# Optimization experiments

Measured on AMD Instinct MI355X. Metric: run time of the kernel, lower is better.

## Reference

```python
import jax, jax.numpy as jnp
import numpy as np


def _gcn_conv(x, edge_index, W, b):
    """Faithful PyG GCNConv: add self-loops, symmetric norm, scatter-sum, bias."""
    n = x.shape[0]
    loop = jnp.arange(n, dtype=edge_index.dtype)
    src = jnp.concatenate([edge_index[0], loop])  # [E+n]
    dst = jnp.concatenate([edge_index[1], loop])
    # in-degree at dst (edge_weight = 1), as in gcn_norm
    deg = jax.ops.segment_sum(jnp.ones(src.shape[0], x.dtype), dst, num_segments=n)
    dinv = jnp.where(deg > 0, jax.lax.rsqrt(deg), 0.0)
    norm = dinv[src] * dinv[dst]                  # [E+n]
    h = x @ W                                     # [n, C] small GEMM
    msg = h[src] * norm[:, None]                  # gather + scale (dominant traffic)
    out = jax.ops.segment_sum(msg, dst, num_segments=n)  # scatter-sum
    return out + b


def setup_inputs() -> dict:
    key = jax.random.key(0)
    ks = jax.random.split(key, 8)
    N, E, C = 50000, 1000000, 64
    scale = 1.0 / np.sqrt(C)
    return {
        "x_star": jax.random.normal(ks[0], (N, C), jnp.float32),
        "x_gal": jax.random.normal(ks[1], (N, C), jnp.float32),
        "edge_ss_near": jax.random.randint(ks[2], (2, E), 0, N, jnp.int64),
        "edge_ss_far": jax.random.randint(ks[3], (2, E), 0, N, jnp.int64),
        "edge_gg_near": jax.random.randint(ks[4], (2, E), 0, N, jnp.int64),
        "W_ss_near": jax.random.normal(ks[5], (C, C), jnp.float32) * scale,
        "W_ss_far": jax.random.normal(ks[6], (C, C), jnp.float32) * scale,
        "W_gg_near": jax.random.normal(ks[7], (C, C), jnp.float32) * scale,
        "b_ss_near": jnp.zeros((C,), jnp.float32),
        "b_ss_far": jnp.zeros((C,), jnp.float32),
        "b_gg_near": jnp.zeros((C,), jnp.float32),
    }


def reference(x_star, x_gal, edge_ss_near, edge_ss_far, edge_gg_near,
              W_ss_near, W_ss_far, W_gg_near,
              b_ss_near, b_ss_far, b_gg_near):
    # HeteroConv with aggr='sum': per-edge-type GCNConv, summed per dst node type.
    out_star = (_gcn_conv(x_star, edge_ss_near, W_ss_near, b_ss_near)
                + _gcn_conv(x_star, edge_ss_far, W_ss_far, b_ss_far))
    out_gal = _gcn_conv(x_gal, edge_gg_near, W_gg_near, b_gg_near)
    return out_star, out_gal
```

## Files before the change

### kernel.cpp

```cpp
#include <hip/hip_runtime.h>
#include <hip/hip_fp16.h>

#define CCH 64
#define RPB 32
#define PCH 8192
#define NBMAX 1568
#define GR 64
#define SG 8
#define STCAP 8192

typedef int int4a __attribute__((ext_vector_type(4), aligned(4)));

__global__ void __launch_bounds__(256) k_hist(const int* __restrict__ e0,
        const int* __restrict__ e1, const int* __restrict__ e2,
        int* __restrict__ H, int* __restrict__ cnt, int E, int NB, int NBLK) {
    int c = blockIdx.y;
    const int* dd = ((c == 0) ? e0 : (c == 1) ? e1 : e2) + E;
    int base = blockIdx.x * PCH;
    int nE = E - base; if (nE > PCH) nE = PCH;
    __shared__ int hist[NBMAX];
    int t = threadIdx.x;
    for (int i = t; i < NB; i += 256) hist[i] = 0;
    __syncthreads();
    for (int k = t * 4; k < nE; k += 1024) {
        if (k + 3 < nE) {
            int4a d = *(const int4a*)(dd + base + k);
            atomicAdd(&hist[d.x >> 5], 1); atomicAdd(&hist[d.y >> 5], 1);
            atomicAdd(&hist[d.z >> 5], 1); atomicAdd(&hist[d.w >> 5], 1);
        } else {
            for (int j = k; j < nE; ++j) atomicAdd(&hist[dd[base + j] >> 5], 1);
        }
    }
    __syncthreads();
    int* Hrow = H + ((size_t)c * NBLK + blockIdx.x) * NB;
    for (int i = t; i < NB; i += 256) {
        int h = hist[i];
        Hrow[i] = h;
        if (h) atomicAdd(&cnt[c * NB + i], h);
    }
}

__global__ void __launch_bounds__(1024) k_bscan(const int* __restrict__ cnt,
        int* __restrict__ bstart, __half* __restrict__ zrow, int NB, int E) {
    int c = blockIdx.x, t = threadIdx.x;
    if (c == 0 && t < 32) ((float*)zrow)[t] = 0.f;
    __shared__ int sm[1024];
    int i0 = 2 * t, i1 = 2 * t + 1;
    int v0 = (i0 < NB) ? cnt[c * NB + i0] : 0;
    int v1 = (i1 < NB) ? cnt[c * NB + i1] : 0;
    sm[t] = v0 + v1;
    __syncthreads();
    #pragma unroll
    for (int off = 1; off < 1024; off <<= 1) {
        int u = (t >= off) ? sm[t - off] : 0;
        __syncthreads();
        sm[t] += u;
        __syncthreads();
    }
    int ex = sm[t] - (v0 + v1);
    if (i0 < NB) bstart[c * (NB + 1) + i0] = ex;
    if (i1 < NB) bstart[c * (NB + 1) + i1] = ex + v0;
    if (t == 0) bstart[c * (NB + 1) + NB] = E;
}

__global__ void __launch_bounds__(256) k_colscan(int* __restrict__ H,
        const int* __restrict__ bstart, int NB, int NBLK) {
    int c = blockIdx.y;
    int b = blockIdx.x * 4 + (threadIdx.x >> 6);
    if (b >= NB) return;
    int l = threadIdx.x & 63;
    int* Hc = H + (size_t)c * NBLK * NB;
    int run = bstart[c * (NB + 1) + b];
    for (int c0 = 0; c0 < NBLK; c0 += 64) {
        int blk = c0 + l;
        int v = (blk < NBLK) ? Hc[(size_t)blk * NB + b] : 0;
        int s = v;
        #pragma unroll
        for (int off = 1; off < 64; off <<= 1) {
            int u = __shfl_up(s, off, 64);
            if (l >= off) s += u;
        }
        if (blk < NBLK) Hc[(size_t)blk * NB + b] = run + s - v;
        run += __shfl(s, 63, 64);
    }
}

__global__ void __launch_bounds__(256) k_part2(const int* __restrict__ e0,
        const int* __restrict__ e1, const int* __restrict__ e2,
        const int* __restrict__ H, const int* __restrict__ bstart,
        unsigned* __restrict__ bdata, int E, int NB, int NBLK) {
    int c = blockIdx.y;
    const int* ed = (c == 0) ? e0 : (c == 1) ? e1 : e2;
    int base = blockIdx.x * PCH;
    int nE = E - base; if (nE > PCH) nE = PCH;
    __shared__ unsigned staged[PCH];
    __shared__ int hist[NBMAX];
    __shared__ int off[NBMAX];
    __shared__ int sm[256];
    int t = threadIdx.x;
    const int* Hcur = H + ((size_t)c * NBLK + blockIdx.x) * NB;
    const int* Hnxt = (blockIdx.x == NBLK - 1) ? (bstart + c * (NB + 1) + 1)
                                               : (Hcur + NB);
    for (int i = t; i < NB; i += 256) {
        int cu = Hcur[i];
        off[i] = cu;
        hist[i] = Hnxt[i] - cu;
    }
    __syncthreads();
    int C = (NB + 255) >> 8;
    int lo = t * C, hi = lo + C; if (hi > NB) hi = NB; if (lo > NB) lo = NB;
    int s = 0;
    for (int i = lo; i < hi; ++i) s += hist[i];
    sm[t] = s;
    __syncthreads();
    #pragma unroll
    for (int o = 1; o < 256; o <<= 1) {
        int u = (t >= o) ? sm[t - o] : 0;
        __syncthreads();
        sm[t] += u;
        __syncthreads();
    }
    int run = (t == 0) ? 0 : sm[t - 1];
    for (int i = lo; i < hi; ++i) {
        int h = hist[i];
        off[i] -= run;
        hist[i] = run;
        run += h;
    }
    __syncthreads();
    for (int k = t * 4; k < nE; k += 1024) {
        if (k + 3 < nE) {
            int4a s4 = *(const int4a*)(ed + base + k);
            int4a d4 = *(const int4a*)(ed + E + base + k);
            int sl;
            sl = atomicAdd(&hist[d4.x >> 5], 1); staged[sl] = (unsigned)s4.x | ((unsigned)d4.x << 16);
            sl = atomicAdd(&hist[d4.y >> 5], 1); staged[sl] = (unsigned)s4.y | ((unsigned)d4.y << 16);
            sl = atomicAdd(&hist[d4.z >> 5], 1); staged[sl] = (unsigned)s4.z | ((unsigned)d4.z << 16);
            sl = atomicAdd(&hist[d4.w >> 5], 1); staged[sl] = (unsigned)s4.w | ((unsigned)d4.w << 16);
        } else {
            for (int j = k; j < nE; ++j) {
                int s0 = ed[base + j];
                int d0 = ed[E + base + j];
                int sl = atomicAdd(&hist[d0 >> 5], 1);
                staged[sl] = (unsigned)s0 | ((unsigned)d0 << 16);
            }
        }
    }
    __syncthreads();
    unsigned* bo = bdata + (size_t)c * E;
    for (int sI = t; sI < nE; sI += 256) {
        unsigned rec = staged[sI];
        int b = (int)(rec >> 16) >> 5;
        bo[off[b] + sI] = rec;
    }
}

__global__ void __launch_bounds__(256) k_sort32(const unsigned* __restrict__ bdata,
        const int* __restrict__ bstart, int* __restrict__ sdat,
        int* __restrict__ rs, float* __restrict__ dinv, int E, int N, int NB) {
    int c = blockIdx.y;
    int b0 = blockIdx.x * SG;
    __shared__ unsigned staged[STCAP];
    __shared__ int cnt[SG * RPB];
    __shared__ int cur[SG * RPB];
    __shared__ int sb[SG + 1];
    int t = threadIdx.x;
    cnt[t] = 0;
    if (t <= SG) {
        int b = b0 + t; if (b > NB) b = NB;
        sb[t] = bstart[c * (NB + 1) + b];
    }
    __syncthreads();
    int s0 = sb[0], sE = sb[SG];
    int n = sE - s0;
    const unsigned* bd = bdata + (size_t)c * E;
    bool fits = (n <= STCAP);
    if (fits) {
        for (int i = t; i < n; i += 256) staged[i] = bd[s0 + i];
        __syncthreads();
        for (int i = t; i < n; i += 256) {
            int dst = (int)(staged[i] >> 16);
            atomicAdd(&cnt[((dst >> 5) - b0) * RPB + (dst & 31)], 1);
        }
    } else {
        for (int i = s0 + t; i < sE; i += 256) {
            int dst = (int)(bd[i] >> 16);
            atomicAdd(&cnt[((dst >> 5) - b0) * RPB + (dst & 31)], 1);
        }
    }
    __syncthreads();
    {
        int v = cnt[t];
        int s = v;
        #pragma unroll
        for (int off = 1; off < RPB; off <<= 1) {
            int u = __shfl_up(s, off, RPB);
            if ((t & (RPB - 1)) >= off) s += u;
        }
        int g = t >> 5, r = t & 31;
        int ex = sb[g] + s - v;
        cur[t] = ex;
        int row = (b0 + g) * RPB + r;
        if (b0 + g < NB && row < N) {
            rs[c * (N + 1) + row] = ex;
            dinv[c * N + row] = rsqrtf((float)(v + 1));
        }
    }
    if (blockIdx.x == 0 && t == 0) rs[c * (N + 1) + N] = E;
    __syncthreads();
    int* so = sdat + (size_t)c * E;
    if (fits) {
        for (int i = t; i < n; i += 256) {
            unsigned r = staged[i];
            int dst = (int)(r >> 16);
            int slot = atomicAdd(&cur[((dst >> 5) - b0) * RPB + (dst & 31)], 1);
            so[slot] = (int)(r & 0xFFFFu);
        }
    } else {
        for (int i = s0 + t; i < sE; i += 256) {
            unsigned r = bd[i];
            int dst = (int)(r >> 16);
            int slot = atomicAdd(&cur[((dst >> 5) - b0) * RPB + (dst & 31)], 1);
            so[slot] = (int)(r & 0xFFFFu);
        }
    }
}

__global__ void __launch_bounds__(256) k_gemm_all(const float* __restrict__ xs_,
        const float* __restrict__ xg_, const float* __restrict__ W0,
        const float* __restrict__ W1, const float* __restrict__ W2,
        const float* __restrict__ dinv, __half* __restrict__ h16, int N) {
    int star = (blockIdx.y == 0);
    const float* x = star ? xs_ : xg_;
    __shared__ float Ws[2][CCH * CCH];
    __shared__ float xT[CCH * (GR + 1)];
    int t = threadIdx.x;
    int row0 = blockIdx.x * GR;
    size_t NC = (size_t)N * CCH;
    if (star) {
        #pragma unroll
        for (int j = 0; j < 4; ++j) {
            int idx = j * 1024 + t * 4;
            *(float4*)(&Ws[0][idx]) = *(const float4*)(W0 + idx);
            *(float4*)(&Ws[1][idx]) = *(const float4*)(W1 + idx);
        }
    } else {
        #pragma unroll
        for (int j = 0; j < 4; ++j) {
            int idx = j * 1024 + t * 4;
            *(float4*)(&Ws[0][idx]) = *(const float4*)(W2 + idx);
        }
    }
    #pragma unroll
    for (int j = 0; j < 4; ++j) {
        int idx = t + j * 256;
        int r = idx >> 4;
        int c0 = (idx & 15) * 4;
        int row = row0 + r;
        float4 v = make_float4(0.f, 0.f, 0.f, 0.f);
        if (row < N) v = *(const float4*)(x + (size_t)row * CCH + c0);
        xT[(c0 + 0) * (GR + 1) + r] = v.x;
        xT[(c0 + 1) * (GR + 1) + r] = v.y;
        xT[(c0 + 2) * (GR + 1) + r] = v.z;
        xT[(c0 + 3) * (GR + 1) + r] = v.w;
    }
    __syncthreads();
    int c4 = (t & 15) * 4;
    int r0 = (t >> 4) * 4;
    if (star) {
        float4 a0 = make_float4(0.f, 0.f, 0.f, 0.f), a1 = a0, a2 = a0, a3 = a0;
        float4 d0 = a0, d1 = a0, d2 = a0, d3 = a0;
        #pragma unroll 4
        for (int k = 0; k < CCH; ++k) {
            float4 wv = *(float4*)(&Ws[0][k * CCH + c4]);
            float4 uv = *(float4*)(&Ws[1][k * CCH + c4]);
            float x0 = xT[k * (GR + 1) + r0 + 0];
            float x1 = xT[k * (GR + 1) + r0 + 1];
            float x2 = xT[k * (GR + 1) + r0 + 2];
            float x3 = xT[k * (GR + 1) + r0 + 3];
            a0.x += x0 * wv.x; a0.y += x0 * wv.y; a0.z += x0 * wv.z; a0.w += x0 * wv.w;
            a1.x += x1 * wv.x; a1.y += x1 * wv.y; a1.z += x1 * wv.z; a1.w += x1 * wv.w;
            a2.x += x2 * wv.x; a2.y += x2 * wv.y; a2.z += x2 * wv.z; a2.w += x2 * wv.w;
            a3.x += x3 * wv.x; a3.y += x3 * wv.y; a3.z += x3 * wv.z; a3.w += x3 * wv.w;
            d0.x += x0 * uv.x; d0.y += x0 * uv.y; d0.z += x0 * uv.z; d0.w += x0 * uv.w;
            d1.x += x1 * uv.x; d1.y += x1 * uv.y; d1.z += x1 * uv.z; d1.w += x1 * uv.w;
            d2.x += x2 * uv.x; d2.y += x2 * uv.y; d2.z += x2 * uv.z; d2.w += x2 * uv.w;
            d3.x += x3 * uv.x; d3.y += x3 * uv.y; d3.z += x3 * uv.z; d3.w += x3 * uv.w;
        }
        float4 av[4] = {a0, a1, a2, a3};
        float4 dv4[4] = {d0, d1, d2, d3};
        #pragma unroll
        for (int i = 0; i < 4; ++i) {
            int row = row0 + r0 + i;
            if (row < N) {
                float dd0 = dinv[row];
                float dd1 = dinv[N + row];
                union { __half2 h2[2]; float2 f2; } u;
                u.h2[0] = __floats2half2_rn(av[i].x * dd0, av[i].y * dd0);
                u.h2[1] = __floats2half2_rn(av[i].z * dd0, av[i].w * dd0);
                *(float2*)(h16 + (size_t)row * CCH + c4) = u.f2;
                u.h2[0] = __floats2half2_rn(dv4[i].x * dd1, dv4[i].y * dd1);
                u.h2[1] = __floats2half2_rn(dv4[i].z * dd1, dv4[i].w * dd1);
                *(float2*)(h16 + NC + (size_t)row * CCH + c4) = u.f2;
            }
        }
    } else {
        float4 a0 = make_float4(0.f, 0.f, 0.f, 0.f), a1 = a0, a2 = a0, a3 = a0;
        #pragma unroll 8
        for (int k = 0; k < CCH; ++k) {
            float4 wv = *(float4*)(&Ws[0][k * CCH + c4]);
            float x0 = xT[k * (GR + 1) + r0 + 0];
            float x1 = xT[k * (GR + 1) + r0 + 1];
            float x2 = xT[k * (GR + 1) + r0 + 2];
            float x3 = xT[k * (GR + 1) + r0 + 3];
            a0.x += x0 * wv.x; a0.y += x0 * wv.y; a0.z += x0 * wv.z; a0.w += x0 * wv.w;
            a1.x += x1 * wv.x; a1.y += x1 * wv.y; a1.z += x1 * wv.z; a1.w += x1 * wv.w;
            a2.x += x2 * wv.x; a2.y += x2 * wv.y; a2.z += x2 * wv.z; a2.w += x2 * wv.w;
            a3.x += x3 * wv.x; a3.y += x3 * wv.y; a3.z += x3 * wv.z; a3.w += x3 * wv.w;
        }
        float4 av[4] = {a0, a1, a2, a3};
        #pragma unroll
        for (int i = 0; i < 4; ++i) {
            int row = row0 + r0 + i;
            if (row < N) {
                float dd = dinv[2 * N + row];
                union { __half2 h2[2]; float2 f2; } u;
                u.h2[0] = __floats2half2_rn(av[i].x * dd, av[i].y * dd);
                u.h2[1] = __floats2half2_rn(av[i].z * dd, av[i].w * dd);
                *(float2*)(h16 + 2 * NC + (size_t)row * CCH + c4) = u.f2;
            }
        }
    }
}

__device__ __forceinline__ float4 gat4p(const __half* __restrict__ p, int l16) {
    union { float2 f2; __half2 h2[2]; } u;
    u.f2 = ((const float2*)p)[l16];
    float2 a = __half22float2(u.h2[0]);
    float2 b = __half22float2(u.h2[1]);
    return make_float4(a.x, a.y, b.x, b.y);
}

__device__ __forceinline__ void acc4(float4& a, float4 v) {
    a.x += v.x; a.y += v.y; a.z += v.z; a.w += v.w;
}

__global__ void __launch_bounds__(256) k_pull(const int* __restrict__ rs,
        const int* __restrict__ sdat, const __half* __restrict__ h16,
        const float* __restrict__ dinv, const __half* __restrict__ zrow,
        const float* __restrict__ b0, const float* __restrict__ b1,
        const float* __restrict__ b2,
        float* __restrict__ out, int N, int E) {
    int row = blockIdx.x * 4 + (threadIdx.x >> 6);
    if (row >= 2 * N) return;
    int lane = threadIdx.x & 63;
    int q = lane >> 4;
    int l16 = lane & 15;
    size_t NC = (size_t)N * CCH;

    const __half* hcL;
    const int* sdL;
    int beg, end;
    float ddL;
    float4 bias;
    float* op;
    float4 acc = make_float4(0.f, 0.f, 0.f, 0.f);
    if (row < N) {
        int cv = q >> 1;
        const int* rsA = rs + cv * (N + 1);
        int bg = rsA[row], eg = rsA[row + 1];
        int mid = (bg + eg) >> 1;
        beg = (q & 1) ? mid : bg;
        end = (q & 1) ? eg : mid;
        hcL = h16 + (size_t)cv * NC;
        sdL = sdat + (size_t)cv * E;
        ddL = dinv[cv * N + row];
        if (!(q & 1)) acc = gat4p(hcL + (size_t)row * CCH, l16);
        float4 bv0 = ((const float4*)b0)[l16];
        float4 bv1 = ((const float4*)b1)[l16];
        bias = make_float4(bv0.x + bv1.x, bv0.y + bv1.y,
                           bv0.z + bv1.z, bv0.w + bv1.w);
        op = out + (size_t)row * CCH;
    } else {
        int r = row - N;
        const int* rs2 = rs + 2 * (N + 1);
        int bg = rs2[r], eg = rs2[r + 1];
        int len = eg - bg;
        beg = bg + ((len * q) >> 2);
        end = bg + ((len * (q + 1)) >> 2);
        hcL = h16 + 2 * NC;
        sdL = sdat + 2 * (size_t)E;
        ddL = dinv[2 * N + r];
        if (q == 0) acc = gat4p(hcL + (size_t)r * CCH, l16);
        bias = ((const float4*)b2)[l16];
        op = out + NC + (size_t)r * CCH;
    }

    int i = beg;
    for (; i + 7 < end; i += 8) {
        int4a q0 = *(const int4a*)(sdL + i);
        int4a q1 = *(const int4a*)(sdL + i + 4);
        float4 v0 = gat4p(hcL + (size_t)q0.x * CCH, l16);
        float4 v1 = gat4p(hcL + (size_t)q0.y * CCH, l16);
        float4 v2 = gat4p(hcL + (size_t)q0.z * CCH, l16);
        float4 v3 = gat4p(hcL + (size_t)q0.w * CCH, l16);
        float4 v4 = gat4p(hcL + (size_t)q1.x * CCH, l16);
        float4 v5 = gat4p(hcL + (size_t)q1.y * CCH, l16);
        float4 v6 = gat4p(hcL + (size_t)q1.z * CCH, l16);
        float4 v7 = gat4p(hcL + (size_t)q1.w * CCH, l16);
        acc4(acc, v0); acc4(acc, v1); acc4(acc, v2); acc4(acc, v3);
        acc4(acc, v4); acc4(acc, v5); acc4(acc, v6); acc4(acc, v7);
    }
    if (i < end) {
        int4a q0 = *(const int4a*)(sdL + i);
        int4a q1 = *(const int4a*)(sdL + i + 4);
        const __half* p0 = hcL + (size_t)q0.x * CCH;
        const __half* p1 = (i + 1 < end) ? hcL + (size_t)q0.y * CCH : zrow;
        const __half* p2 = (i + 2 < end) ? hcL + (size_t)q0.z * CCH : zrow;
        const __half* p3 = (i + 3 < end) ? hcL + (size_t)q0.w * CCH : zrow;
        const __half* p4 = (i + 4 < end) ? hcL + (size_t)q1.x * CCH : zrow;
        const __half* p5 = (i + 5 < end) ? hcL + (size_t)q1.y * CCH : zrow;
        const __half* p6 = (i + 6 < end) ? hcL + (size_t)q1.z * CCH : zrow;
        const __half* p7 = (i + 7 < end) ? hcL + (size_t)q1.w * CCH : zrow;
        float4 v0 = gat4p(p0, l16);
        float4 v1 = gat4p(p1, l16);
        float4 v2 = gat4p(p2, l16);
        float4 v3 = gat4p(p3, l16);
        float4 v4 = gat4p(p4, l16);
        float4 v5 = gat4p(p5, l16);
        float4 v6 = gat4p(p6, l16);
        float4 v7 = gat4p(p7, l16);
        acc4(acc, v0); acc4(acc, v1); acc4(acc, v2); acc4(acc, v3);
        acc4(acc, v4); acc4(acc, v5); acc4(acc, v6); acc4(acc, v7);
    }

    float4 t;
    t.x = acc.x * ddL; t.y = acc.y * ddL; t.z = acc.z * ddL; t.w = acc.w * ddL;
    t.x += __shfl_xor(t.x, 16, 64); t.y += __shfl_xor(t.y, 16, 64);
    t.z += __shfl_xor(t.z, 16, 64); t.w += __shfl_xor(t.w, 16, 64);
    t.x += __shfl_xor(t.x, 32, 64); t.y += __shfl_xor(t.y, 32, 64);
    t.z += __shfl_xor(t.z, 32, 64); t.w += __shfl_xor(t.w, 32, 64);
    if (lane < 16) {
        t.x += bias.x; t.y += bias.y; t.z += bias.z; t.w += bias.w;
        ((float4*)op)[l16] = t;
    }
}

static inline size_t align256(size_t x) { return (x + 255) & ~(size_t)255; }

extern "C" void kernel_launch(void* const* d_in, const int* in_sizes, int n_in,
                              void* d_out, int out_size, void* d_ws, size_t ws_size,
                              hipStream_t stream) {
    const float* x_star = (const float*)d_in[0];
    const float* x_gal  = (const float*)d_in[1];
    const int*   e_ssn  = (const int*)d_in[2];
    const int*   e_ssf  = (const int*)d_in[3];
    const int*   e_ggn  = (const int*)d_in[4];
    const float* W_ssn  = (const float*)d_in[5];
    const float* W_ssf  = (const float*)d_in[6];
    const float* W_ggn  = (const float*)d_in[7];
    const float* b_ssn  = (const float*)d_in[8];
    const float* b_ssf  = (const float*)d_in[9];
    const float* b_ggn  = (const float*)d_in[10];

    const int N  = in_sizes[0] / CCH;
    const int E  = in_sizes[2] / 2;
    const size_t NC = (size_t)N * CCH;
    const int NB   = (N + RPB - 1) / RPB;
    const int NBLK = (E + PCH - 1) / PCH;

    char* w = (char*)d_ws;
    __half*   h16    = (__half*)w;   w += align256((size_t)3 * NC * 2);
    float*    dinv   = (float*)w;    w += align256((size_t)3 * N * 4);
    unsigned* bdata  = (unsigned*)w; w += align256((size_t)3 * E * 4);
    int*      sdat   = (int*)w;      w += align256((size_t)3 * E * 4);
    int*      H      = (int*)w;      w += align256((size_t)3 * NBLK * NB * 4);
    int*      cnt    = (int*)w;      w += align256((size_t)3 * NB * 4);
    int*      bstart = (int*)w;      w += align256((size_t)3 * (NB + 1) * 4);
    int*      rs     = (int*)w;      w += align256((size_t)3 * (N + 1) * 4);
    __half*   zrow   = (__half*)w;   w += align256((size_t)CCH * 2);

    const int B = 256;

    hipMemsetAsync(cnt, 0, (size_t)3 * NB * 4, stream);
    k_hist<<<dim3(NBLK, 3), B, 0, stream>>>(e_ssn, e_ssf, e_ggn, H, cnt, E, NB, NBLK);
    k_bscan<<<3, 1024, 0, stream>>>(cnt, bstart, zrow, NB, E);
    k_colscan<<<dim3((NB + 3) / 4, 3), B, 0, stream>>>(H, bstart, NB, NBLK);
    k_part2<<<dim3(NBLK, 3), B, 0, stream>>>(e_ssn, e_ssf, e_ggn, H, bstart,
                                             bdata, E, NB, NBLK);
    k_sort32<<<dim3((NB + SG - 1) / SG, 3), B, 0, stream>>>(bdata, bstart, sdat,
                                                            rs, dinv, E, N, NB);
    k_gemm_all<<<dim3((N + GR - 1) / GR, 2), B, 0, stream>>>(x_star, x_gal,
                                                             W_ssn, W_ssf, W_ggn,
                                                             dinv, h16, N);
    k_pull<<<(2 * N + 3) / 4, B, 0, stream>>>(rs, sdat, h16, dinv, zrow,
                                              b_ssn, b_ssf, b_ggn,
                                              (float*)d_out, N, E);
}
```

Baseline: 232.9 us.

## Halve partition chunk and sort groups; derive bucket totals from column scan

Removes the global atomic bucket counters and their memset: k_colscan now scans the per-block histograms from zero and writes column totals, k_bscan scans those totals, and k_part2 adds the bucket start when computing offsets. The partition chunk size (PCH) and sort group size (SG/STCAP) are halved, so more blocks are launched with smaller shared-memory staging, which should improve occupancy and load balance. The cost is a larger histogram matrix H to scan, more blocks, and k_sort32 leaving half its threads idle during the per-row scan.

```diff
diff --git a/kernel.cpp b/kernel.cpp
--- a/kernel.cpp
+++ b/kernel.cpp
@@ -3,17 +3,17 @@
 
 #define CCH 64
 #define RPB 32
-#define PCH 8192
+#define PCH 4096
 #define NBMAX 1568
 #define GR 64
-#define SG 8
-#define STCAP 8192
+#define SG 4
+#define STCAP 4096
 
 typedef int int4a __attribute__((ext_vector_type(4), aligned(4)));
 
 __global__ void __launch_bounds__(256) k_hist(const int* __restrict__ e0,
         const int* __restrict__ e1, const int* __restrict__ e2,
-        int* __restrict__ H, int* __restrict__ cnt, int E, int NB, int NBLK) {
+        int* __restrict__ H, int E, int NB, int NBLK) {
     int c = blockIdx.y;
     const int* dd = ((c == 0) ? e0 : (c == 1) ? e1 : e2) + E;
     int base = blockIdx.x * PCH;
@@ -33,21 +33,40 @@
     }
     __syncthreads();
     int* Hrow = H + ((size_t)c * NBLK + blockIdx.x) * NB;
-    for (int i = t; i < NB; i += 256) {
-        int h = hist[i];
-        Hrow[i] = h;
-        if (h) atomicAdd(&cnt[c * NB + i], h);
-    }
-}
-
-__global__ void __launch_bounds__(1024) k_bscan(const int* __restrict__ cnt,
+    for (int i = t; i < NB; i += 256) Hrow[i] = hist[i];
+}
+
+__global__ void __launch_bounds__(256) k_colscan(int* __restrict__ H,
+        int* __restrict__ colsum, int NB, int NBLK) {
+    int c = blockIdx.y;
+    int b = blockIdx.x * 4 + (threadIdx.x >> 6);
+    if (b >= NB) return;
+    int l = threadIdx.x & 63;
+    int* Hc = H + (size_t)c * NBLK * NB;
+    int run = 0;
+    for (int c0 = 0; c0 < NBLK; c0 += 64) {
+        int blk = c0 + l;
+        int v = (blk < NBLK) ? Hc[(size_t)blk * NB + b] : 0;
+        int s = v;
+        #pragma unroll
+        for (int off = 1; off < 64; off <<= 1) {
+            int u = __shfl_up(s, off, 64);
+            if (l >= off) s += u;
+        }
+        if (blk < NBLK) Hc[(size_t)blk * NB + b] = run + s - v;
+        run += __shfl(s, 63, 64);
+    }
+    if (l == 0) colsum[c * NB + b] = run;
+}
+
+__global__ void __launch_bounds__(1024) k_bscan(const int* __restrict__ colsum,
         int* __restrict__ bstart, __half* __restrict__ zrow, int NB, int E) {
     int c = blockIdx.x, t = threadIdx.x;
     if (c == 0 && t < 32) ((float*)zrow)[t] = 0.f;
     __shared__ int sm[1024];
     int i0 = 2 * t, i1 = 2 * t + 1;
-    int v0 = (i0 < NB) ? cnt[c * NB + i0] : 0;
-    int v1 = (i1 < NB) ? cnt[c * NB + i1] : 0;
+    int v0 = (i0 < NB) ? colsum[c * NB + i0] : 0;
+    int v1 = (i1 < NB) ? colsum[c * NB + i1] : 0;
     sm[t] = v0 + v1;
     __syncthreads();
     #pragma unroll
@@ -63,31 +82,10 @@
     if (t == 0) bstart[c * (NB + 1) + NB] = E;
 }
 
-__global__ void __launch_bounds__(256) k_colscan(int* __restrict__ H,
-        const int* __restrict__ bstart, int NB, int NBLK) {
-    int c = blockIdx.y;
-    int b = blockIdx.x * 4 + (threadIdx.x >> 6);
-    if (b >= NB) return;
-    int l = threadIdx.x & 63;
-    int* Hc = H + (size_t)c * NBLK * NB;
-    int run = bstart[c * (NB + 1) + b];
-    for (int c0 = 0; c0 < NBLK; c0 += 64) {
-        int blk = c0 + l;
-        int v = (blk < NBLK) ? Hc[(size_t)blk * NB + b] : 0;
-        int s = v;
-        #pragma unroll
-        for (int off = 1; off < 64; off <<= 1) {
-            int u = __shfl_up(s, off, 64);
-            if (l >= off) s += u;
-        }
-        if (blk < NBLK) Hc[(size_t)blk * NB + b] = run + s - v;
-        run += __shfl(s, 63, 64);
-    }
-}
-
 __global__ void __launch_bounds__(256) k_part2(const int* __restrict__ e0,
         const int* __restrict__ e1, const int* __restrict__ e2,
-        const int* __restrict__ H, const int* __restrict__ bstart,
+        const int* __restrict__ H, const int* __restrict__ colsum,
+        const int* __restrict__ bstart,
         unsigned* __restrict__ bdata, int E, int NB, int NBLK) {
     int c = blockIdx.y;
     const int* ed = (c == 0) ? e0 : (c == 1) ? e1 : e2;
@@ -99,11 +97,12 @@
     __shared__ int sm[256];
     int t = threadIdx.x;
     const int* Hcur = H + ((size_t)c * NBLK + blockIdx.x) * NB;
-    const int* Hnxt = (blockIdx.x == NBLK - 1) ? (bstart + c * (NB + 1) + 1)
+    const int* Hnxt = (blockIdx.x == NBLK - 1) ? (colsum + c * NB)
                                                : (Hcur + NB);
+    const int* bs = bstart + c * (NB + 1);
     for (int i = t; i < NB; i += 256) {
         int cu = Hcur[i];
-        off[i] = cu;
+        off[i] = bs[i] + cu;
         hist[i] = Hnxt[i] - cu;
     }
     __syncthreads();
@@ -165,7 +164,7 @@
     __shared__ int cur[SG * RPB];
     __shared__ int sb[SG + 1];
     int t = threadIdx.x;
-    cnt[t] = 0;
+    if (t < SG * RPB) cnt[t] = 0;
     if (t <= SG) {
         int b = b0 + t; if (b > NB) b = NB;
         sb[t] = bstart[c * (NB + 1) + b];
@@ -189,7 +188,7 @@
         }
     }
     __syncthreads();
-    {
+    if (t < SG * RPB) {
         int v = cnt[t];
         int s = v;
         #pragma unroll
@@ -475,19 +474,18 @@
     unsigned* bdata  = (unsigned*)w; w += align256((size_t)3 * E * 4);
     int*      sdat   = (int*)w;      w += align256((size_t)3 * E * 4);
     int*      H      = (int*)w;      w += align256((size_t)3 * NBLK * NB * 4);
-    int*      cnt    = (int*)w;      w += align256((size_t)3 * NB * 4);
+    int*      colsum = (int*)w;      w += align256((size_t)3 * NB * 4);
     int*      bstart = (int*)w;      w += align256((size_t)3 * (NB + 1) * 4);
     int*      rs     = (int*)w;      w += align256((size_t)3 * (N + 1) * 4);
     __half*   zrow   = (__half*)w;   w += align256((size_t)CCH * 2);
 
     const int B = 256;
 
-    hipMemsetAsync(cnt, 0, (size_t)3 * NB * 4, stream);
-    k_hist<<<dim3(NBLK, 3), B, 0, stream>>>(e_ssn, e_ssf, e_ggn, H, cnt, E, NB, NBLK);
-    k_bscan<<<3, 1024, 0, stream>>>(cnt, bstart, zrow, NB, E);
-    k_colscan<<<dim3((NB + 3) / 4, 3), B, 0, stream>>>(H, bstart, NB, NBLK);
-    k_part2<<<dim3(NBLK, 3), B, 0, stream>>>(e_ssn, e_ssf, e_ggn, H, bstart,
-                                             bdata, E, NB, NBLK);
+    k_hist<<<dim3(NBLK, 3), B, 0, stream>>>(e_ssn, e_ssf, e_ggn, H, E, NB, NBLK);
+    k_colscan<<<dim3((NB + 3) / 4, 3), B, 0, stream>>>(H, colsum, NB, NBLK);
+    k_bscan<<<3, 1024, 0, stream>>>(colsum, bstart, zrow, NB, E);
+    k_part2<<<dim3(NBLK, 3), B, 0, stream>>>(e_ssn, e_ssf, e_ggn, H, colsum,
+                                             bstart, bdata, E, NB, NBLK);
     k_sort32<<<dim3((NB + SG - 1) / SG, 3), B, 0, stream>>>(bdata, bstart, sdat,
                                                             rs, dinv, E, N, NB);
     k_gemm_all<<<dim3((N + GR - 1) / GR, 2), B, 0, stream>>>(x_star, x_gal,
```

Result: slower. 237.7 us (+2.1%).

## Widen counting-sort buckets to 256 rows and split pull into two launches

Applied to the files above, without the earlier changes.

Changes the two-level counting sort of edges by destination from 32-row buckets to 256-row buckets. Each k_sort32 block now owns one bucket, and per-thread loops over the bucket histogram collapse to one bucket per thread. The first-pass histograms shrink, so the per-chunk H matrix and the scans over it get smaller. The pull kernel is split into two launches, star rows then galaxy rows, via a row offset. Larger buckets give fewer sort blocks with more work each, and bucket sizes (about 5k edges) still fit the STCAP staging buffer.

```diff
diff --git a/kernel.cpp b/kernel.cpp
--- a/kernel.cpp
+++ b/kernel.cpp
@@ -2,11 +2,10 @@
 #include <hip/hip_fp16.h>
 
 #define CCH 64
-#define RPB 32
+#define BKT 256
 #define PCH 8192
-#define NBMAX 1568
+#define NBMAX 200
 #define GR 64
-#define SG 8
 #define STCAP 8192
 
 typedef int int4a __attribute__((ext_vector_type(4), aligned(4)));
@@ -20,23 +19,23 @@
     int nE = E - base; if (nE > PCH) nE = PCH;
     __shared__ int hist[NBMAX];
     int t = threadIdx.x;
-    for (int i = t; i < NB; i += 256) hist[i] = 0;
+    if (t < NB) hist[t] = 0;
     __syncthreads();
     for (int k = t * 4; k < nE; k += 1024) {
         if (k + 3 < nE) {
             int4a d = *(const int4a*)(dd + base + k);
-            atomicAdd(&hist[d.x >> 5], 1); atomicAdd(&hist[d.y >> 5], 1);
-            atomicAdd(&hist[d.z >> 5], 1); atomicAdd(&hist[d.w >> 5], 1);
+            atomicAdd(&hist[d.x >> 8], 1); atomicAdd(&hist[d.y >> 8], 1);
+            atomicAdd(&hist[d.z >> 8], 1); atomicAdd(&hist[d.w >> 8], 1);
         } else {
-            for (int j = k; j < nE; ++j) atomicAdd(&hist[dd[base + j] >> 5], 1);
+            for (int j = k; j < nE; ++j) atomicAdd(&hist[dd[base + j] >> 8], 1);
         }
     }
     __syncthreads();
     int* Hrow = H + ((size_t)c * NBLK + blockIdx.x) * NB;
-    for (int i = t; i < NB; i += 256) {
-        int h = hist[i];
-        Hrow[i] = h;
-        if (h) atomicAdd(&cnt[c * NB + i], h);
+    if (t < NB) {
+        int h = hist[t];
+        Hrow[t] = h;
+        if (h) atomicAdd(&cnt[c * NB + t], h);
     }
 }
 
@@ -101,16 +100,13 @@
     const int* Hcur = H + ((size_t)c * NBLK + blockIdx.x) * NB;
     const int* Hnxt = (blockIdx.x == NBLK - 1) ? (bstart + c * (NB + 1) + 1)
                                                : (Hcur + NB);
-    for (int i = t; i < NB; i += 256) {
-        int cu = Hcur[i];
-        off[i] = cu;
-        hist[i] = Hnxt[i] - cu;
-    }
-    __syncthreads();
-    int C = (NB + 255) >> 8;
-    int lo = t * C, hi = lo + C; if (hi > NB) hi = NB; if (lo > NB) lo = NB;
-    int s = 0;
-    for (int i = lo; i < hi; ++i) s += hist[i];
+    if (t < NB) {
+        int cu = Hcur[t];
+        off[t] = cu;
+        hist[t] = Hnxt[t] - cu;
+    }
+    __syncthreads();
+    int s = (t < NB) ? hist[t] : 0;
     sm[t] = s;
     __syncthreads();
     #pragma unroll
@@ -120,12 +116,10 @@
         sm[t] += u;
         __syncthreads();
     }
-    int run = (t == 0) ? 0 : sm[t - 1];
-    for (int i = lo; i < hi; ++i) {
-        int h = hist[i];
-        off[i] -= run;
-        hist[i] = run;
-        run += h;
+    if (t < NB) {
+        int run = sm[t] - s;
+        off[t] -= run;
+        hist[t] = run;
     }
     __syncthreads();
     for (int k = t * 4; k < nE; k += 1024) {
@@ -133,15 +127,15 @@
             int4a s4 = *(const int4a*)(ed + base + k);
             int4a d4 = *(const int4a*)(ed + E + base + k);
             int sl;
-            sl = atomicAdd(&hist[d4.x >> 5], 1); staged[sl] = (unsigned)s4.x | ((unsigned)d4.x << 16);
-            sl = atomicAdd(&hist[d4.y >> 5], 1); staged[sl] = (unsigned)s4.y | ((unsigned)d4.y << 16);
-            sl = atomicAdd(&hist[d4.z >> 5], 1); staged[sl] = (unsigned)s4.z | ((unsigned)d4.z << 16);
-            sl = atomicAdd(&hist[d4.w >> 5], 1); staged[sl] = (unsigned)s4.w | ((unsigned)d4.w << 16);
+            sl = atomicAdd(&hist[d4.x >> 8], 1); staged[sl] = (unsigned)s4.x | ((unsigned)d4.x << 16);
+            sl = atomicAdd(&hist[d4.y >> 8], 1); staged[sl] = (unsigned)s4.y | ((unsigned)d4.y << 16);
+            sl = atomicAdd(&hist[d4.z >> 8], 1); staged[sl] = (unsigned)s4.z | ((unsigned)d4.z << 16);
+            sl = atomicAdd(&hist[d4.w >> 8], 1); staged[sl] = (unsigned)s4.w | ((unsigned)d4.w << 16);
         } else {
             for (int j = k; j < nE; ++j) {
                 int s0 = ed[base + j];
                 int d0 = ed[E + base + j];
-                int sl = atomicAdd(&hist[d0 >> 5], 1);
+                int sl = atomicAdd(&hist[d0 >> 8], 1);
                 staged[sl] = (unsigned)s0 | ((unsigned)d0 << 16);
             }
         }
@@ -150,7 +144,7 @@
     unsigned* bo = bdata + (size_t)c * E;
     for (int sI = t; sI < nE; sI += 256) {
         unsigned rec = staged[sI];
-        int b = (int)(rec >> 16) >> 5;
+        int b = (int)(rec >> 16) >> 8;
         bo[off[b] + sI] = rec;
     }
 }
@@ -159,68 +153,62 @@
         const int* __restrict__ bstart, int* __restrict__ sdat,
         int* __restrict__ rs, float* __restrict__ dinv, int E, int N, int NB) {
     int c = blockIdx.y;
-    int b0 = blockIdx.x * SG;
+    int b = blockIdx.x;
     __shared__ unsigned staged[STCAP];
-    __shared__ int cnt[SG * RPB];
-    __shared__ int cur[SG * RPB];
-    __shared__ int sb[SG + 1];
+    __shared__ int cnt[BKT];
+    __shared__ int cur[BKT];
+    __shared__ int wsum[4];
     int t = threadIdx.x;
     cnt[t] = 0;
-    if (t <= SG) {
-        int b = b0 + t; if (b > NB) b = NB;
-        sb[t] = bstart[c * (NB + 1) + b];
-    }
-    __syncthreads();
-    int s0 = sb[0], sE = sb[SG];
+    __syncthreads();
+    int s0 = bstart[c * (NB + 1) + b];
+    int sE = bstart[c * (NB + 1) + b + 1];
     int n = sE - s0;
     const unsigned* bd = bdata + (size_t)c * E;
     bool fits = (n <= STCAP);
     if (fits) {
         for (int i = t; i < n; i += 256) staged[i] = bd[s0 + i];
         __syncthreads();
-        for (int i = t; i < n; i += 256) {
-            int dst = (int)(staged[i] >> 16);
-            atomicAdd(&cnt[((dst >> 5) - b0) * RPB + (dst & 31)], 1);
-        }
+        for (int i = t; i < n; i += 256)
+            atomicAdd(&cnt[(staged[i] >> 16) & 255], 1);
     } else {
-        for (int i = s0 + t; i < sE; i += 256) {
-            int dst = (int)(bd[i] >> 16);
-            atomicAdd(&cnt[((dst >> 5) - b0) * RPB + (dst & 31)], 1);
-        }
-    }
-    __syncthreads();
-    {
-        int v = cnt[t];
-        int s = v;
-        #pragma unroll
-        for (int off = 1; off < RPB; off <<= 1) {
-            int u = __shfl_up(s, off, RPB);
-            if ((t & (RPB - 1)) >= off) s += u;
-        }
-        int g = t >> 5, r = t & 31;
-        int ex = sb[g] + s - v;
-        cur[t] = ex;
-        int row = (b0 + g) * RPB + r;
-        if (b0 + g < NB && row < N) {
-            rs[c * (N + 1) + row] = ex;
-            dinv[c * N + row] = rsqrtf((float)(v + 1));
-        }
-    }
-    if (blockIdx.x == 0 && t == 0) rs[c * (N + 1) + N] = E;
+        for (int i = s0 + t; i < sE; i += 256)
+            atomicAdd(&cnt[(bd[i] >> 16) & 255], 1);
+    }
+    __syncthreads();
+    int v = cnt[t];
+    int s = v;
+    #pragma unroll
+    for (int off = 1; off < 64; off <<= 1) {
+        int u = __shfl_up(s, off, 64);
+        if ((t & 63) >= off) s += u;
+    }
+    int w = t >> 6;
+    if ((t & 63) == 63) wsum[w] = s;
+    __syncthreads();
+    int wpre = 0;
+    #pragma unroll
+    for (int j = 0; j < 4; ++j) if (j < w) wpre += wsum[j];
+    int ex = s0 + wpre + s - v;
+    cur[t] = ex;
+    int row = b * BKT + t;
+    if (row < N) {
+        rs[c * (N + 1) + row] = ex;
+        dinv[c * N + row] = rsqrtf((float)(v + 1));
+    }
+    if (b == 0 && t == 0) rs[c * (N + 1) + N] = E;
     __syncthreads();
     int* so = sdat + (size_t)c * E;
     if (fits) {
         for (int i = t; i < n; i += 256) {
             unsigned r = staged[i];
-            int dst = (int)(r >> 16);
-            int slot = atomicAdd(&cur[((dst >> 5) - b0) * RPB + (dst & 31)], 1);
+            int slot = atomicAdd(&cur[(r >> 16) & 255], 1);
             so[slot] = (int)(r & 0xFFFFu);
         }
     } else {
         for (int i = s0 + t; i < sE; i += 256) {
             unsigned r = bd[i];
-            int dst = (int)(r >> 16);
-            int slot = atomicAdd(&cur[((dst >> 5) - b0) * RPB + (dst & 31)], 1);
+            int slot = atomicAdd(&cur[(r >> 16) & 255], 1);
             so[slot] = (int)(r & 0xFFFFu);
         }
     }
@@ -350,8 +338,8 @@
         const float* __restrict__ dinv, const __half* __restrict__ zrow,
         const float* __restrict__ b0, const float* __restrict__ b1,
         const float* __restrict__ b2,
-        float* __restrict__ out, int N, int E) {
-    int row = blockIdx.x * 4 + (threadIdx.x >> 6);
+        float* __restrict__ out, int N, int E, int row0) {
+    int row = row0 + blockIdx.x * 4 + (threadIdx.x >> 6);
     if (row >= 2 * N) return;
     int lane = threadIdx.x & 63;
     int q = lane >> 4;
@@ -466,7 +454,7 @@
     const int N  = in_sizes[0] / CCH;
     const int E  = in_sizes[2] / 2;
     const size_t NC = (size_t)N * CCH;
-    const int NB   = (N + RPB - 1) / RPB;
+    const int NB   = (N + BKT - 1) / BKT;
     const int NBLK = (E + PCH - 1) / PCH;
 
     char* w = (char*)d_ws;
@@ -488,12 +476,14 @@
     k_colscan<<<dim3((NB + 3) / 4, 3), B, 0, stream>>>(H, bstart, NB, NBLK);
     k_part2<<<dim3(NBLK, 3), B, 0, stream>>>(e_ssn, e_ssf, e_ggn, H, bstart,
                                              bdata, E, NB, NBLK);
-    k_sort32<<<dim3((NB + SG - 1) / SG, 3), B, 0, stream>>>(bdata, bstart, sdat,
-                                                            rs, dinv, E, N, NB);
+    k_sort32<<<dim3(NB, 3), B, 0, stream>>>(bdata, bstart, sdat, rs, dinv, E, N, NB);
     k_gemm_all<<<dim3((N + GR - 1) / GR, 2), B, 0, stream>>>(x_star, x_gal,
                                                              W_ssn, W_ssf, W_ggn,
                                                              dinv, h16, N);
-    k_pull<<<(2 * N + 3) / 4, B, 0, stream>>>(rs, sdat, h16, dinv, zrow,
-                                              b_ssn, b_ssf, b_ggn,
-                                              (float*)d_out, N, E);
-}
+    k_pull<<<(N + 3) / 4, B, 0, stream>>>(rs, sdat, h16, dinv, zrow,
+                                          b_ssn, b_ssf, b_ggn,
+                                          (float*)d_out, N, E, 0);
+    k_pull<<<(N + 3) / 4, B, 0, stream>>>(rs, sdat, h16, dinv, zrow,
+                                          b_ssn, b_ssf, b_ggn,
+                                          (float*)d_out, N, E, N);
+}
```

Measured after the change: 234.0 us. No clear change (+0.5%).
